# Performance work log

Measured on AMD Instinct MI355X. Metric: run time of the kernel, lower is better.

## Reference

```python
import jax, jax.numpy as jnp
import numpy as np

P = 16           # patch size
E = P * P        # embed dim of MHA (must equal dim)
NH = 4           # num heads
HD = E // NH     # head dim


def setup_inputs() -> dict:
    key = jax.random.key(0)
    k1, k2, k3, k4, k5 = jax.random.split(key, 5)
    B, C, H, W = 2, 256, 256, 256
    scale = 1.0 / np.sqrt(E)
    return {
        "x": jax.random.normal(k1, (B, C, H, W), dtype=jnp.float32),
        "w_in": jax.random.normal(k2, (3 * E, E), dtype=jnp.float32) * scale,
        "b_in": jnp.zeros((3 * E,), dtype=jnp.float32),
        "w_out": jax.random.normal(k3, (E, E), dtype=jnp.float32) * scale,
        "b_out": jnp.zeros((E,), dtype=jnp.float32),
    }


def reference(x, w_in, b_in, w_out, b_out):
    B, C, H, W = x.shape
    nP = (H // P) * (W // P)
    # x.unfold(2,p,p).unfold(3,p,p).reshape(B,C,-1,p*p)
    patches = (
        x.reshape(B, C, H // P, P, W // P, P)
        .transpose(0, 1, 2, 4, 3, 5)
        .reshape(B, C, nP, E)
    )
    # permute(0,2,1,3).reshape(B*nP, C, p*p): batch=B*nP, seq=C, embed=E
    t = patches.transpose(0, 2, 1, 3).reshape(B * nP, C, E)

    qkv = t @ w_in.T + b_in                      # (N, C, 3E)
    q, k, v = jnp.split(qkv, 3, axis=-1)

    def to_heads(a):  # (N, C, E) -> (N, NH, C, HD)
        return a.reshape(B * nP, C, NH, HD).transpose(0, 2, 1, 3)

    q, k, v = to_heads(q), to_heads(k), to_heads(v)
    scores = jnp.einsum("nhqd,nhkd->nhqk", q * (HD ** -0.5), k)
    attn = jax.nn.softmax(scores, axis=-1)
    o = jnp.einsum("nhqk,nhkd->nhqd", attn, v)   # (N, NH, C, HD)
    o = o.transpose(0, 2, 1, 3).reshape(B * nP, C, E)
    o = o @ w_out.T + b_out
    # reshape(B, -1, C, p*p).permute(0, 2, 1, 3)
    return o.reshape(B, nP, C, E).transpose(0, 2, 1, 3)
```

## Files before the change

### kernel.cpp

```cpp
#include <hip/hip_runtime.h>
#include <hip/hip_bf16.h>

typedef __attribute__((ext_vector_type(8))) short s16x8;
typedef __attribute__((ext_vector_type(4))) float f32x4;

#define WS_SEG 67108864ULL

#if defined(__has_attribute)
#if __has_attribute(amdgpu_num_vgpr)
#define VGPR_CAP_128 __attribute__((amdgpu_num_vgpr(128)))
#else
#define VGPR_CAP_128
#endif
#else
#define VGPR_CAP_128
#endif

static __device__ __forceinline__ unsigned short f2bf(float f) {
    return __builtin_bit_cast(unsigned short, __float2bfloat16(f));
}
static __device__ __forceinline__ unsigned int pack2(float a, float b) {
    return (unsigned int)f2bf(a) | ((unsigned int)f2bf(b) << 16);
}
static __device__ __forceinline__ s16x8 u4cast(uint4 u) {
    return __builtin_bit_cast(s16x8, u);
}
static __device__ __forceinline__ void gl_lds16(const void* g, void* l) {
    __builtin_amdgcn_global_load_lds(
        (const __attribute__((address_space(1))) unsigned int*)g,
        (__attribute__((address_space(3))) unsigned int*)l, 16, 0, 0);
}

__global__ __launch_bounds__(256) void convw_swz(const float* __restrict__ wi,
                                                 unsigned short* __restrict__ wb) {
    int i = (blockIdx.x * 256 + threadIdx.x) * 4;
    float4 v = *reinterpret_cast<const float4*>(wi + i);
    int bb = i * 2;
    int row = i >> 8;
    int dst = (bb & ~127) | ((bb & 127) ^ ((row & 7) << 4));
    uint2 o = { pack2(v.x, v.y), pack2(v.z, v.w) };
    *reinterpret_cast<uint2*>((char*)wb + dst) = o;
}

__global__ __launch_bounds__(256) void gather_swz(const float* __restrict__ x,
                                                  unsigned short* __restrict__ t) {
    int q = (blockIdx.x * 256 + threadIdx.x) * 4;
    int e = q & 255, c = (q >> 8) & 255, n = q >> 16;
    int b = n >> 8, p = n & 255;
    int xi = ((b * 256 + c) * 256 + (p >> 4) * 16 + (e >> 4)) * 256 + (p & 15) * 16 + (e & 15);
    float4 v = *reinterpret_cast<const float4*>(x + xi);
    int bb = q * 2;
    int row = q >> 8;
    int dst = (bb & ~127) | ((bb & 127) ^ ((row & 7) << 4));
    uint2 o = { pack2(v.x, v.y), pack2(v.z, v.w) };
    *reinterpret_cast<uint2*>((char*)t + dst) = o;
}

template<int MODE>
__global__ __launch_bounds__(256) void gemm3(
    const unsigned short* __restrict__ A,
    const unsigned short* __restrict__ Wb,
    const float* __restrict__ bias,
    unsigned short* __restrict__ Qo, unsigned short* __restrict__ Ko,
    unsigned short* __restrict__ Vt, float* __restrict__ Out)
{
    __shared__ __align__(16) char smem[32768];
    char* AsB = smem;
    char* BsB = smem + 16384;

    const int t = threadIdx.x, w = t >> 6, lane = t & 63;
    const int lr = lane & 15, lk = lane >> 4;
    const int wm = w >> 1, wn = w & 1;

    constexpr int NB = (MODE == 0) ? 6 : 2;
    const int flat = blockIdx.x;
    const int xcd = flat & 7, idx = flat >> 3;
    const int bm = xcd * 128 + idx / NB;
    const int bn = idx % NB;

    f32x4 acc[4][4] = {};

    const char* Ag = (const char*)A + (size_t)bm * 65536;
    const char* Bg = (const char*)Wb + (size_t)bn * 65536;

    for (int kk = 0; kk < 4; ++kk) {
        #pragma unroll
        for (int i = 0; i < 4; ++i) {
            int u = (i * 4 + w) * 64 + lane;
            int row = u >> 3, cb = (u & 7) * 16;
            gl_lds16(Ag + row * 512 + kk * 128 + cb, AsB + (i * 4 + w) * 1024);
            gl_lds16(Bg + row * 512 + kk * 128 + cb, BsB + (i * 4 + w) * 1024);
        }
        __syncthreads();
        #pragma unroll
        for (int kc = 0; kc < 2; ++kc) {
            s16x8 af[4], bf[4];
            #pragma unroll
            for (int fm = 0; fm < 4; ++fm) {
                int r = wm * 64 + fm * 16 + lr;
                af[fm] = *reinterpret_cast<const s16x8*>(
                    AsB + r * 128 + ((kc * 64 + lk * 16) ^ ((r & 7) << 4)));
            }
            #pragma unroll
            for (int fn = 0; fn < 4; ++fn) {
                int cc = wn * 64 + fn * 16 + lr;
                bf[fn] = *reinterpret_cast<const s16x8*>(
                    BsB + cc * 128 + ((kc * 64 + lk * 16) ^ ((cc & 7) << 4)));
            }
            __builtin_amdgcn_s_setprio(1);
            #pragma unroll
            for (int fm = 0; fm < 4; ++fm)
                #pragma unroll
                for (int fn = 0; fn < 4; ++fn)
                    acc[fm][fn] = __builtin_amdgcn_mfma_f32_16x16x32_bf16(af[fm], bf[fn], acc[fm][fn], 0, 0, 0);
            __builtin_amdgcn_s_setprio(0);
        }
        __syncthreads();
    }

    if (MODE == 1) {
        #pragma unroll
        for (int fn = 0; fn < 4; ++fn) {
            int colg = bn * 128 + wn * 64 + fn * 16 + lr;
            float bv = bias[colg];
            #pragma unroll
            for (int fm = 0; fm < 4; ++fm)
                #pragma unroll
                for (int j = 0; j < 4; ++j) {
                    int rg = bm * 128 + wm * 64 + fm * 16 + lk * 4 + j;
                    int n = rg >> 8, c = rg & 255;
                    int b = n >> 8, p = n & 255;
                    Out[(((b * 256 + c) * 256 + p) << 8) + colg] = acc[fm][fn][j] + bv;
                }
        }
        return;
    }

    unsigned short* T = (unsigned short*)smem;
    const int X = bn >> 1;
    const int h0 = (bn & 1) * 2;
    const int n = bm >> 1;

    #pragma unroll
    for (int fn = 0; fn < 4; ++fn) {
        int col_local = wn * 64 + fn * 16 + lr;
        float bv = bias[bn * 128 + col_local];
        #pragma unroll
        for (int fm = 0; fm < 4; ++fm)
            #pragma unroll
            for (int j = 0; j < 4; ++j) {
                int c_local = wm * 64 + fm * 16 + lk * 4 + j;
                unsigned short hv = f2bf(acc[fm][fn][j] + bv);
                if (X < 2) {
                    *reinterpret_cast<unsigned short*>(
                        (char*)T + c_local * 256 + col_local * 2) = hv;
                } else {
                    int hl = col_local >> 6, d = col_local & 63;
                    *reinterpret_cast<unsigned short*>(
                        (char*)T + hl * 16384 + d * 256 + ((c_local * 2) ^ ((d & 7) << 4))) = hv;
                }
            }
    }
    __syncthreads();

    if (X < 2) {
        unsigned short* base = (X == 0) ? Qo : Ko;
        #pragma unroll
        for (int i = 0; i < 8; ++i) {
            int u = i * 256 + t;
            int c_local = u >> 4;
            int cbyte = (u & 15) * 16;
            int h = h0 + (cbyte >> 7);
            int db = cbyte & 127;
            uint4 vv = *reinterpret_cast<const uint4*>((char*)T + u * 16);
            int c = (bm & 1) * 128 + c_local;
            *reinterpret_cast<uint4*>(
                (char*)base + (size_t)((n * 4 + h) * 256 + c) * 128 + db) = vv;
        }
    } else {
        #pragma unroll
        for (int i = 0; i < 8; ++i) {
            int u = i * 256 + t;
            int rowr = u >> 4;
            int hl = rowr >> 6, d = rowr & 63;
            int cb2 = (u & 15) * 16;
            int c2 = cb2 ^ ((d & 7) << 4);
            uint4 vv = *reinterpret_cast<const uint4*>((char*)T + u * 16);
            *reinterpret_cast<uint4*>(
                (char*)Vt + (size_t)((n * 4 + h0 + hl) * 64 + d) * 512 + (bm & 1) * 256 + c2) = vv;
        }
    }
}

__global__ __launch_bounds__(512) VGPR_CAP_128 void attn6(
    const unsigned short* __restrict__ Q,
    const unsigned short* __restrict__ K,
    const unsigned short* __restrict__ V,
    unsigned short* __restrict__ O)
{
    __shared__ __align__(16) char KsB[32768];
    __shared__ __align__(16) char VsB[32768];
    __shared__ __align__(16) char OtrB[8][2048];

    const int nh = blockIdx.x;
    const int n = nh >> 2, h = nh & 3;
    const int t = threadIdx.x, w = t >> 6, lane = t & 63;
    const int lr = lane & 15, lk = lane >> 4;

    const unsigned short* Qg = Q + (size_t)nh * 16384;
    const char* Kg = (const char*)K + (size_t)nh * 32768;
    const char* Vg = (const char*)V + (size_t)nh * 32768;

    #pragma unroll
    for (int i = 0; i < 4; ++i) {
        int u = i * 512 + t;
        int row = u >> 3, cb = (u & 7) * 16;
        uint4 val = *reinterpret_cast<const uint4*>(Kg + u * 16);
        *reinterpret_cast<uint4*>(KsB + row * 128 + (cb ^ ((row & 7) << 4))) = val;
    }
    #pragma unroll
    for (int i = 0; i < 4; ++i) {
        int u = i * 512 + t;
        int row = u >> 5, cb = (u & 31) * 16;
        uint4 val = *reinterpret_cast<const uint4*>(Vg + u * 16);
        *reinterpret_cast<uint4*>(VsB + row * 512 + (cb ^ ((row & 7) << 4))) = val;
    }
    __syncthreads();

    const float sc = 0.125f * 1.44269504f;
    const int swz = (lr & 7) << 4;

    #pragma unroll
    for (int it = 0; it < 2; ++it) {
        const int qt = w * 2 + it;

        s16x8 bq0 = *reinterpret_cast<const s16x8*>(Qg + (qt * 16 + lr) * 64 + lk * 8);
        s16x8 bq1 = *reinterpret_cast<const s16x8*>(Qg + (qt * 16 + lr) * 64 + 32 + lk * 8);

        f32x4 s[16];
        #pragma unroll
        for (int kt = 0; kt < 16; ++kt) {
            const int rb = (kt * 16 + lr) * 128;
            s16x8 a0 = *reinterpret_cast<const s16x8*>(KsB + rb + ((lk * 16) ^ swz));
            s16x8 a1 = *reinterpret_cast<const s16x8*>(KsB + rb + ((64 + lk * 16) ^ swz));
            f32x4 z = { 0.f, 0.f, 0.f, 0.f };
            __builtin_amdgcn_s_setprio(1);
            z = __builtin_amdgcn_mfma_f32_16x16x32_bf16(a0, bq0, z, 0, 0, 0);
            z = __builtin_amdgcn_mfma_f32_16x16x32_bf16(a1, bq1, z, 0, 0, 0);
            __builtin_amdgcn_s_setprio(0);
            s[kt] = z;
        }

        float m8[8];
        #pragma unroll
        for (int i = 0; i < 8; ++i) {
            float a = fmaxf(fmaxf(s[i][0], s[i][1]), fmaxf(s[i][2], s[i][3]));
            float b = fmaxf(fmaxf(s[i + 8][0], s[i + 8][1]), fmaxf(s[i + 8][2], s[i + 8][3]));
            m8[i] = fmaxf(a, b);
        }
        float m = fmaxf(fmaxf(fmaxf(m8[0], m8[1]), fmaxf(m8[2], m8[3])),
                        fmaxf(fmaxf(m8[4], m8[5]), fmaxf(m8[6], m8[7])));
        m = fmaxf(m, __shfl_xor(m, 16));
        m = fmaxf(m, __shfl_xor(m, 32));

        const float nb = -m * sc;
        float lp[8];
        s16x8 pf[8];
        #pragma unroll
        for (int kb = 0; kb < 8; ++kb) {
            float p0 = exp2f(__builtin_fmaf(s[2 * kb][0], sc, nb));
            float p1 = exp2f(__builtin_fmaf(s[2 * kb][1], sc, nb));
            float p2 = exp2f(__builtin_fmaf(s[2 * kb][2], sc, nb));
            float p3 = exp2f(__builtin_fmaf(s[2 * kb][3], sc, nb));
            float p4 = exp2f(__builtin_fmaf(s[2 * kb + 1][0], sc, nb));
            float p5 = exp2f(__builtin_fmaf(s[2 * kb + 1][1], sc, nb));
            float p6 = exp2f(__builtin_fmaf(s[2 * kb + 1][2], sc, nb));
            float p7 = exp2f(__builtin_fmaf(s[2 * kb + 1][3], sc, nb));
            lp[kb] = ((p0 + p1) + (p2 + p3)) + ((p4 + p5) + (p6 + p7));
            uint4 pk = { pack2(p0, p1), pack2(p2, p3), pack2(p4, p5), pack2(p6, p7) };
            pf[kb] = u4cast(pk);
        }
        float l = ((lp[0] + lp[1]) + (lp[2] + lp[3])) + ((lp[4] + lp[5]) + (lp[6] + lp[7]));
        l += __shfl_xor(l, 16);
        l += __shfl_xor(l, 32);

        f32x4 oacc[4] = {};
        #pragma unroll
        for (int kb = 0; kb < 8; ++kb) {
            #pragma unroll
            for (int dt = 0; dt < 4; ++dt) {
                const char* vb = VsB + (dt * 16 + lr) * 512;
                uint2 v0 = *reinterpret_cast<const uint2*>(vb + ((kb * 64 + lk * 8) ^ swz));
                uint2 v1 = *reinterpret_cast<const uint2*>(vb + ((kb * 64 + lk * 8 + 32) ^ swz));
                uint4 uu = { v0.x, v0.y, v1.x, v1.y };
                __builtin_amdgcn_s_setprio(1);
                oacc[dt] = __builtin_amdgcn_mfma_f32_16x16x32_bf16(u4cast(uu), pf[kb], oacc[dt], 0, 0, 0);
                __builtin_amdgcn_s_setprio(0);
            }
        }

        const float rl = 1.0f / l;
        char* ob = OtrB[w];
        #pragma unroll
        for (int dt = 0; dt < 4; ++dt) {
            unsigned int w0 = pack2(oacc[dt][0] * rl, oacc[dt][1] * rl);
            unsigned int w1 = pack2(oacc[dt][2] * rl, oacc[dt][3] * rl);
            int cb0 = dt * 32 + lk * 8;
            *reinterpret_cast<unsigned int*>(ob + lr * 128 + (cb0 ^ swz)) = w0;
            *reinterpret_cast<unsigned int*>(ob + lr * 128 + ((cb0 + 4) ^ swz)) = w1;
        }
        #pragma unroll
        for (int pp = 0; pp < 2; ++pp) {
            int qrow = lane >> 2;
            int cbX = (lane & 3) * 32 + pp * 16;
            uint4 vv = *reinterpret_cast<const uint4*>(ob + qrow * 128 + cbX);
            *reinterpret_cast<uint4*>(
                (char*)O + (size_t)(n * 256 + qt * 16 + qrow) * 512 + h * 128 + cbX) = vv;
        }
    }
}

extern "C" void kernel_launch(void* const* d_in, const int* in_sizes, int n_in,
                              void* d_out, int out_size, void* d_ws, size_t ws_size,
                              hipStream_t stream) {
    const float* x     = (const float*)d_in[0];
    const float* w_in  = (const float*)d_in[1];
    const float* b_in  = (const float*)d_in[2];
    const float* w_out = (const float*)d_in[3];
    const float* b_out = (const float*)d_in[4];

    char* ws = (char*)d_ws;
    unsigned short* tO = (unsigned short*)(ws);
    unsigned short* Qw = (unsigned short*)(ws + WS_SEG);
    unsigned short* Kw = (unsigned short*)(ws + 2 * WS_SEG);
    unsigned short* Vw = (unsigned short*)(ws + 3 * WS_SEG);

    unsigned short* WbIn = (unsigned short*)((float*)d_out + out_size - 98304);

    convw_swz<<<192, 256, 0, stream>>>(w_in, WbIn);
    gather_swz<<<32768, 256, 0, stream>>>(x, tO);

    gemm3<0><<<6144, 256, 0, stream>>>(tO, WbIn, b_in, Qw, Kw, Vw, nullptr);

    attn6<<<2048, 512, 0, stream>>>(Qw, Kw, Vw, tO);

    unsigned short* WbOut = Kw;
    convw_swz<<<64, 256, 0, stream>>>(w_out, WbOut);

    gemm3<1><<<2048, 256, 0, stream>>>(tO, WbOut, b_out,
                                       nullptr, nullptr, nullptr, (float*)d_out);
}
```

Baseline: 304.6 us.

## Fuse patch gather into QKV GEMM and double-buffer weight tiles

Removes the separate gather_swz pass, so the QKV GEMM reads fp32 patches straight from x, converts them to bf16 in registers and writes them swizzled into LDS. The B (weight) tile gets a second LDS buffer, and A loads for the next k-step are issued before the MFMAs of the current one, overlapping global loads with compute. This saves a full write and re-read of the bf16 patch tensor. In exchange, each of the six N-blocks now re-reads fp32 x (twice the bytes of bf16), LDS grows to 48KB, and register pressure rises, which may lower occupancy. The output GEMM now stages A through registers instead of direct global-to-LDS loads.

```diff
diff --git a/kernel.cpp b/kernel.cpp
--- a/kernel.cpp
+++ b/kernel.cpp
@@ -42,31 +42,18 @@
     *reinterpret_cast<uint2*>((char*)wb + dst) = o;
 }
 
-__global__ __launch_bounds__(256) void gather_swz(const float* __restrict__ x,
-                                                  unsigned short* __restrict__ t) {
-    int q = (blockIdx.x * 256 + threadIdx.x) * 4;
-    int e = q & 255, c = (q >> 8) & 255, n = q >> 16;
-    int b = n >> 8, p = n & 255;
-    int xi = ((b * 256 + c) * 256 + (p >> 4) * 16 + (e >> 4)) * 256 + (p & 15) * 16 + (e & 15);
-    float4 v = *reinterpret_cast<const float4*>(x + xi);
-    int bb = q * 2;
-    int row = q >> 8;
-    int dst = (bb & ~127) | ((bb & 127) ^ ((row & 7) << 4));
-    uint2 o = { pack2(v.x, v.y), pack2(v.z, v.w) };
-    *reinterpret_cast<uint2*>((char*)t + dst) = o;
-}
-
 template<int MODE>
-__global__ __launch_bounds__(256) void gemm3(
-    const unsigned short* __restrict__ A,
+__global__ __launch_bounds__(256) void gemm4(
+    const float* __restrict__ Xf,
+    const unsigned short* __restrict__ Ab,
     const unsigned short* __restrict__ Wb,
     const float* __restrict__ bias,
     unsigned short* __restrict__ Qo, unsigned short* __restrict__ Ko,
     unsigned short* __restrict__ Vt, float* __restrict__ Out)
 {
-    __shared__ __align__(16) char smem[32768];
+    __shared__ __align__(16) char smem[49152];
     char* AsB = smem;
-    char* BsB = smem + 16384;
+    char* BsB0 = smem + 16384;
 
     const int t = threadIdx.x, w = t >> 6, lane = t & 63;
     const int lr = lane & 15, lk = lane >> 4;
@@ -78,20 +65,81 @@
     const int bm = xcd * 128 + idx / NB;
     const int bn = idx % NB;
 
-    f32x4 acc[4][4] = {};
-
-    const char* Ag = (const char*)A + (size_t)bm * 65536;
+    const float* xrow = nullptr;
+    const char* Arow = nullptr;
+    if (MODE == 0) {
+        const int r = t >> 1;
+        const int n_ = bm >> 1;
+        const int b_ = n_ >> 8, p_ = n_ & 255;
+        const int c_ = (bm & 1) * 128 + r;
+        xrow = Xf + (((size_t)(b_ * 256 + c_) * 256 + (p_ >> 4) * 16) * 256
+                     + (p_ & 15) * 16);
+    } else {
+        Arow = (const char*)Ab + (size_t)bm * 65536;
+    }
     const char* Bg = (const char*)Wb + (size_t)bn * 65536;
 
-    for (int kk = 0; kk < 4; ++kk) {
+    float4 fa[4][2];
+    uint4  ua[4];
+
+    auto loadA = [&](int kk) {
+        if (MODE == 0) {
+            #pragma unroll
+            for (int s = 0; s < 4; ++s) {
+                int eg = kk * 64 + (t & 1) * 32 + s * 8;
+                const float* p = xrow + (eg >> 4) * 256 + (eg & 15);
+                fa[s][0] = *reinterpret_cast<const float4*>(p);
+                fa[s][1] = *reinterpret_cast<const float4*>(p + 4);
+            }
+        } else {
+            #pragma unroll
+            for (int i = 0; i < 4; ++i) {
+                int u = i * 256 + t;
+                int row = u >> 3, cb = (u & 7) * 16;
+                ua[i] = *reinterpret_cast<const uint4*>(Arow + row * 512 + kk * 128 + cb);
+            }
+        }
+    };
+    auto writeA = [&]() {
+        if (MODE == 0) {
+            const int r = t >> 1;
+            const int swzr = (r & 7) << 4;
+            #pragma unroll
+            for (int s = 0; s < 4; ++s) {
+                uint4 pk = { pack2(fa[s][0].x, fa[s][0].y), pack2(fa[s][0].z, fa[s][0].w),
+                             pack2(fa[s][1].x, fa[s][1].y), pack2(fa[s][1].z, fa[s][1].w) };
+                int cb = (t & 1) * 64 + s * 16;
+                *reinterpret_cast<uint4*>(AsB + r * 128 + (cb ^ swzr)) = pk;
+            }
+        } else {
+            #pragma unroll
+            for (int i = 0; i < 4; ++i) {
+                int u = i * 256 + t;
+                int row = u >> 3, cb = (u & 7) * 16;
+                *reinterpret_cast<uint4*>(AsB + row * 128 + cb) = ua[i];
+            }
+        }
+    };
+    auto stageB = [&](int kk) {
+        char* dst = BsB0 + (kk & 1) * 16384;
         #pragma unroll
         for (int i = 0; i < 4; ++i) {
             int u = (i * 4 + w) * 64 + lane;
             int row = u >> 3, cb = (u & 7) * 16;
-            gl_lds16(Ag + row * 512 + kk * 128 + cb, AsB + (i * 4 + w) * 1024);
-            gl_lds16(Bg + row * 512 + kk * 128 + cb, BsB + (i * 4 + w) * 1024);
-        }
+            gl_lds16(Bg + row * 512 + kk * 128 + cb, dst + (i * 4 + w) * 1024);
+        }
+    };
+
+    f32x4 acc[4][4] = {};
+
+    loadA(0);
+    stageB(0);
+
+    for (int kk = 0; kk < 4; ++kk) {
+        writeA();
         __syncthreads();
+        if (kk < 3) { loadA(kk + 1); stageB(kk + 1); }
+        const char* Bcur = BsB0 + (kk & 1) * 16384;
         #pragma unroll
         for (int kc = 0; kc < 2; ++kc) {
             s16x8 af[4], bf[4];
@@ -105,7 +153,7 @@
             for (int fn = 0; fn < 4; ++fn) {
                 int cc = wn * 64 + fn * 16 + lr;
                 bf[fn] = *reinterpret_cast<const s16x8*>(
-                    BsB + cc * 128 + ((kc * 64 + lk * 16) ^ ((cc & 7) << 4)));
+                    Bcur + cc * 128 + ((kc * 64 + lk * 16) ^ ((cc & 7) << 4)));
             }
             __builtin_amdgcn_s_setprio(1);
             #pragma unroll
@@ -115,7 +163,7 @@
                     acc[fm][fn] = __builtin_amdgcn_mfma_f32_16x16x32_bf16(af[fm], bf[fn], acc[fm][fn], 0, 0, 0);
             __builtin_amdgcn_s_setprio(0);
         }
-        __syncthreads();
+        if (kk < 3) __syncthreads();
     }
 
     if (MODE == 1) {
@@ -136,6 +184,7 @@
         return;
     }
 
+    __syncthreads();
     unsigned short* T = (unsigned short*)smem;
     const int X = bn >> 1;
     const int h0 = (bn & 1) * 2;
@@ -338,15 +387,15 @@
     unsigned short* WbIn = (unsigned short*)((float*)d_out + out_size - 98304);
 
     convw_swz<<<192, 256, 0, stream>>>(w_in, WbIn);
-    gather_swz<<<32768, 256, 0, stream>>>(x, tO);
-
-    gemm3<0><<<6144, 256, 0, stream>>>(tO, WbIn, b_in, Qw, Kw, Vw, nullptr);
+
+    gemm4<0><<<6144, 256, 0, stream>>>(x, nullptr, WbIn, b_in,
+                                       Qw, Kw, Vw, nullptr);
 
     attn6<<<2048, 512, 0, stream>>>(Qw, Kw, Vw, tO);
 
     unsigned short* WbOut = Kw;
     convw_swz<<<64, 256, 0, stream>>>(w_out, WbOut);
 
-    gemm3<1><<<2048, 256, 0, stream>>>(tO, WbOut, b_out,
+    gemm4<1><<<2048, 256, 0, stream>>>(nullptr, tO, WbOut, b_out,
                                        nullptr, nullptr, nullptr, (float*)d_out);
 }
```

Result: slower. 374.2 us (+22.9%).

## Split QKV GEMM and store epilogues directly from registers without LDS staging

Applied to the files above, without the earlier changes.

The fused QKV projection is split into two launches: one for Q/K and one for V. The Q/K launch swaps the MFMA operands so each lane holds four consecutive head-dim values, which it stores as packed bf16 uint2 with a vectorized bias load. V and the output projection likewise write straight from accumulators as 8-byte or 16-byte vector stores, removing the LDS transpose round-trip and its barrier. setprio hints and the final-iteration sync are also dropped. Risks are narrower, less coalesced global stores, and the V write no longer applies the XOR swizzle the previous layout used, which the attention kernel may depend on.

```diff
diff --git a/kernel.cpp b/kernel.cpp
--- a/kernel.cpp
+++ b/kernel.cpp
@@ -57,8 +57,8 @@
 }
 
 template<int MODE>
-__global__ __launch_bounds__(256) void gemm3(
-    const unsigned short* __restrict__ A,
+__global__ __launch_bounds__(256) void gemm6(
+    const unsigned short* __restrict__ Ab,
     const unsigned short* __restrict__ Wb,
     const float* __restrict__ bias,
     unsigned short* __restrict__ Qo, unsigned short* __restrict__ Ko,
@@ -72,16 +72,16 @@
     const int lr = lane & 15, lk = lane >> 4;
     const int wm = w >> 1, wn = w & 1;
 
-    constexpr int NB = (MODE == 0) ? 6 : 2;
+    constexpr int NB = (MODE == 0) ? 4 : 2;
     const int flat = blockIdx.x;
     const int xcd = flat & 7, idx = flat >> 3;
     const int bm = xcd * 128 + idx / NB;
     const int bn = idx % NB;
 
+    const char* Ag = (const char*)Ab + (size_t)bm * 65536;
+    const char* Bg = (const char*)Wb + (size_t)bn * 65536;
+
     f32x4 acc[4][4] = {};
-
-    const char* Ag = (const char*)A + (size_t)bm * 65536;
-    const char* Bg = (const char*)Wb + (size_t)bn * 65536;
 
     for (int kk = 0; kk < 4; ++kk) {
         #pragma unroll
@@ -107,87 +107,68 @@
                 bf[fn] = *reinterpret_cast<const s16x8*>(
                     BsB + cc * 128 + ((kc * 64 + lk * 16) ^ ((cc & 7) << 4)));
             }
-            __builtin_amdgcn_s_setprio(1);
             #pragma unroll
             for (int fm = 0; fm < 4; ++fm)
                 #pragma unroll
-                for (int fn = 0; fn < 4; ++fn)
-                    acc[fm][fn] = __builtin_amdgcn_mfma_f32_16x16x32_bf16(af[fm], bf[fn], acc[fm][fn], 0, 0, 0);
-            __builtin_amdgcn_s_setprio(0);
-        }
-        __syncthreads();
-    }
-
-    if (MODE == 1) {
+                for (int fn = 0; fn < 4; ++fn) {
+                    if (MODE == 1)
+                        acc[fm][fn] = __builtin_amdgcn_mfma_f32_16x16x32_bf16(af[fm], bf[fn], acc[fm][fn], 0, 0, 0);
+                    else
+                        acc[fm][fn] = __builtin_amdgcn_mfma_f32_16x16x32_bf16(bf[fn], af[fm], acc[fm][fn], 0, 0, 0);
+                }
+        }
+        if (kk < 3) __syncthreads();
+    }
+
+    const int n = bm >> 1;
+
+    if (MODE == 0) {
+        unsigned short* base = (bn >> 1) ? Ko : Qo;
+        const int h0 = (bn & 1) * 2;
         #pragma unroll
         for (int fn = 0; fn < 4; ++fn) {
-            int colg = bn * 128 + wn * 64 + fn * 16 + lr;
-            float bv = bias[colg];
-            #pragma unroll
-            for (int fm = 0; fm < 4; ++fm)
-                #pragma unroll
-                for (int j = 0; j < 4; ++j) {
-                    int rg = bm * 128 + wm * 64 + fm * 16 + lk * 4 + j;
-                    int n = rg >> 8, c = rg & 255;
-                    int b = n >> 8, p = n & 255;
-                    Out[(((b * 256 + c) * 256 + p) << 8) + colg] = acc[fm][fn][j] + bv;
-                }
-        }
-        return;
-    }
-
-    unsigned short* T = (unsigned short*)smem;
-    const int X = bn >> 1;
-    const int h0 = (bn & 1) * 2;
-    const int n = bm >> 1;
-
-    #pragma unroll
-    for (int fn = 0; fn < 4; ++fn) {
-        int col_local = wn * 64 + fn * 16 + lr;
-        float bv = bias[bn * 128 + col_local];
-        #pragma unroll
-        for (int fm = 0; fm < 4; ++fm)
-            #pragma unroll
-            for (int j = 0; j < 4; ++j) {
-                int c_local = wm * 64 + fm * 16 + lk * 4 + j;
-                unsigned short hv = f2bf(acc[fm][fn][j] + bv);
-                if (X < 2) {
-                    *reinterpret_cast<unsigned short*>(
-                        (char*)T + c_local * 256 + col_local * 2) = hv;
-                } else {
-                    int hl = col_local >> 6, d = col_local & 63;
-                    *reinterpret_cast<unsigned short*>(
-                        (char*)T + hl * 16384 + d * 256 + ((c_local * 2) ^ ((d & 7) << 4))) = hv;
-                }
-            }
-    }
-    __syncthreads();
-
-    if (X < 2) {
-        unsigned short* base = (X == 0) ? Qo : Ko;
-        #pragma unroll
-        for (int i = 0; i < 8; ++i) {
-            int u = i * 256 + t;
-            int c_local = u >> 4;
-            int cbyte = (u & 15) * 16;
-            int h = h0 + (cbyte >> 7);
-            int db = cbyte & 127;
-            uint4 vv = *reinterpret_cast<const uint4*>((char*)T + u * 16);
-            int c = (bm & 1) * 128 + c_local;
-            *reinterpret_cast<uint4*>(
-                (char*)base + (size_t)((n * 4 + h) * 256 + c) * 128 + db) = vv;
+            int col_local = wn * 64 + fn * 16 + lk * 4;
+            f32x4 bv4 = *reinterpret_cast<const f32x4*>(bias + bn * 128 + col_local);
+            int h = h0 + (col_local >> 6), d0 = col_local & 63;
+            #pragma unroll
+            for (int fm = 0; fm < 4; ++fm) {
+                int c = (bm & 1) * 128 + wm * 64 + fm * 16 + lr;
+                uint2 st = { pack2(acc[fm][fn][0] + bv4[0], acc[fm][fn][1] + bv4[1]),
+                             pack2(acc[fm][fn][2] + bv4[2], acc[fm][fn][3] + bv4[3]) };
+                *reinterpret_cast<uint2*>(
+                    (char*)base + (size_t)((n * 4 + h) * 256 + c) * 128 + d0 * 2) = st;
+            }
+        }
+    } else if (MODE == 1) {
+        const int h0 = bn * 2;
+        #pragma unroll
+        for (int fn = 0; fn < 4; ++fn) {
+            int col_local = wn * 64 + fn * 16 + lr;
+            float bv = bias[bn * 128 + col_local];
+            int hl = col_local >> 6, d = col_local & 63;
+            #pragma unroll
+            for (int fm = 0; fm < 4; ++fm) {
+                int c = (bm & 1) * 128 + wm * 64 + fm * 16 + lk * 4;
+                uint2 st = { pack2(acc[fm][fn][0] + bv, acc[fm][fn][1] + bv),
+                             pack2(acc[fm][fn][2] + bv, acc[fm][fn][3] + bv) };
+                *reinterpret_cast<uint2*>(
+                    (char*)Vt + (size_t)((n * 4 + h0 + hl) * 64 + d) * 512 + c * 2) = st;
+            }
         }
     } else {
         #pragma unroll
-        for (int i = 0; i < 8; ++i) {
-            int u = i * 256 + t;
-            int rowr = u >> 4;
-            int hl = rowr >> 6, d = rowr & 63;
-            int cb2 = (u & 15) * 16;
-            int c2 = cb2 ^ ((d & 7) << 4);
-            uint4 vv = *reinterpret_cast<const uint4*>((char*)T + u * 16);
-            *reinterpret_cast<uint4*>(
-                (char*)Vt + (size_t)((n * 4 + h0 + hl) * 64 + d) * 512 + (bm & 1) * 256 + c2) = vv;
+        for (int fn = 0; fn < 4; ++fn) {
+            int colg = bn * 128 + wn * 64 + fn * 16 + lk * 4;
+            f32x4 bv4 = *reinterpret_cast<const f32x4*>(bias + colg);
+            #pragma unroll
+            for (int fm = 0; fm < 4; ++fm) {
+                int rg = bm * 128 + wm * 64 + fm * 16 + lr;
+                int nn = rg >> 8, c = rg & 255;
+                int b = nn >> 8, p = nn & 255;
+                f32x4 st = acc[fm][fn] + bv4;
+                *reinterpret_cast<f32x4*>(
+                    Out + (((size_t)(b * 256 + c) * 256 + p) << 8) + colg) = st;
+            }
         }
     }
 }
@@ -340,13 +321,15 @@
     convw_swz<<<192, 256, 0, stream>>>(w_in, WbIn);
     gather_swz<<<32768, 256, 0, stream>>>(x, tO);
 
-    gemm3<0><<<6144, 256, 0, stream>>>(tO, WbIn, b_in, Qw, Kw, Vw, nullptr);
+    gemm6<0><<<4096, 256, 0, stream>>>(tO, WbIn, b_in, Qw, Kw, nullptr, nullptr);
+    gemm6<1><<<2048, 256, 0, stream>>>(tO, WbIn + 512 * 256, b_in + 512,
+                                       nullptr, nullptr, Vw, nullptr);
 
     attn6<<<2048, 512, 0, stream>>>(Qw, Kw, Vw, tO);
 
     unsigned short* WbOut = Kw;
     convw_swz<<<64, 256, 0, stream>>>(w_out, WbOut);
 
-    gemm3<1><<<2048, 256, 0, stream>>>(tO, WbOut, b_out,
+    gemm6<2><<<2048, 256, 0, stream>>>(tO, WbOut, b_out,
                                        nullptr, nullptr, nullptr, (float*)d_out);
 }
```

New measurement: 297.9 us. 2.2% less time.
